# Kernel tuning notes

Hardware: AMD Instinct MI355X
Metric: run time of the kernel (lower is better)

## Reference

```python
import jax, jax.numpy as jnp
import numpy as np

EPS = 1e-12  # torch F.normalize default eps


def _l2_normalize(x):
    # normalize along last dim, matching F.normalize(dim=2)
    norm = jnp.linalg.norm(x, axis=-1, keepdims=True)
    return x / jnp.maximum(norm, EPS)


def _poly_kernel_mean(a, b):
    # mean over (B,C,C) of squared inner products along T.
    # Original does broadcast (B,1,C,T)*(B,C,1,T) then sum; einsum is the
    # efficient batched-matmul form of the same math.
    g = jnp.einsum('bct,bdt->bcd', a, b)  # (B,C,C)
    return jnp.mean(g * g)


def setup_inputs() -> dict:
    key = jax.random.key(0)
    k1, k2 = jax.random.split(key)
    B, C, T = 16, 128, 16384
    f_s = jax.random.normal(k1, (B, C, T), dtype=jnp.float32)
    f_t = jax.random.normal(k2, (B, C, T), dtype=jnp.float32)
    return {"f_s": f_s, "f_t": f_t}


def reference(f_s, f_t):
    # equal T -> no interpolation branch; view(B,C,-1) is identity for 3D
    s = _l2_normalize(f_s)
    t = _l2_normalize(f_t)
    loss = (jax.lax.stop_gradient(_poly_kernel_mean(t, t))
            + _poly_kernel_mean(s, s)
            - 2.0 * _poly_kernel_mean(s, t))
    return loss
```

## Files before the change

### kernel.cpp

```cpp
#include <hip/hip_runtime.h>
#include <hip/hip_bf16.h>

#define BATCH  16
#define CCH    128
#define TDIM   16384
#define MROWS  256
#define NCHUNK 16
#define KC     (TDIM / NCHUNK)
#define BK     32
#define NSTEP  (KC / BK)
#define PIPE   4
#define BUFFB  32768u
#define LDSBYTES (PIPE * BUFFB)
#define GRAM   (MROWS * MROWS)

typedef __attribute__((ext_vector_type(8))) short bf16x8;
typedef __attribute__((ext_vector_type(4))) float f32x4;
typedef const __attribute__((address_space(1))) unsigned int* gptr_t;
typedef __attribute__((address_space(3))) unsigned int* lptr_t;


__device__ __forceinline__ void issue_stage(
    char* smraw, const float* const (&gsrc)[4], int tid, int stage)
{
  unsigned base = (unsigned)(stage & (PIPE - 1)) * BUFFB;
  #pragma unroll
  for (int j = 0; j < 4; ++j) {
    const float* g = gsrc[j] + (size_t)stage * BK;
    char* l = smraw + base + (unsigned)(j * 512 + tid) * 16u;
    __builtin_amdgcn_global_load_lds((gptr_t)g, (lptr_t)l, 16, 0, 0);
  }
}

__device__ __forceinline__ bf16x8 frag_from_f32(const float* bp, int row, int lhi) {
  const int r7 = row & 7;
  const f32x4* pr = (const f32x4*)(bp + row * 32);
  f32x4 lo = pr[(2 * lhi)     ^ r7];
  f32x4 hi = pr[(2 * lhi + 1) ^ r7];
  union { unsigned u[4]; bf16x8 v; } o;
  asm("v_cvt_pk_bf16_f32 %0, %1, %2" : "=v"(o.u[0]) : "v"(lo.x), "v"(lo.y));
  asm("v_cvt_pk_bf16_f32 %0, %1, %2" : "=v"(o.u[1]) : "v"(lo.z), "v"(lo.w));
  asm("v_cvt_pk_bf16_f32 %0, %1, %2" : "=v"(o.u[2]) : "v"(hi.x), "v"(hi.y));
  asm("v_cvt_pk_bf16_f32 %0, %1, %2" : "=v"(o.u[3]) : "v"(hi.z), "v"(hi.w));
  return o.v;
}

__device__ __forceinline__ void compute_step(
    const float* bp, f32x4 (&acc)[4][8], int wr, int wc, int llo, int lhi)
{
  bf16x8 af[4], bfr[8];
  #pragma unroll
  for (int i = 0; i < 4; ++i)
    af[i] = frag_from_f32(bp, wr * 64 + i * 16 + llo, lhi);
  #pragma unroll
  for (int j = 0; j < 8; ++j)
    bfr[j] = frag_from_f32(bp, wc * 128 + j * 16 + llo, lhi);
  #pragma unroll
  for (int i = 0; i < 4; ++i)
    #pragma unroll
    for (int j = 0; j < 8; ++j)
      acc[i][j] = __builtin_amdgcn_mfma_f32_16x16x32_bf16(af[i], bfr[j], acc[i][j], 0, 0, 0);
}

__global__ __launch_bounds__(512, 2) void gram_kernel(
    const float* __restrict__ fs, const float* __restrict__ ft,
    float* __restrict__ outp, int atomic_mode)
{
  extern __shared__ __attribute__((aligned(16))) char smraw[];

  const int tid   = threadIdx.x;
  const int bidx  = blockIdx.x;
  const int b     = bidx / NCHUNK;
  const int chunk = bidx - b * NCHUNK;
  const int kbase = chunk * KC;

  const int lane = tid & 63;
  const int w    = tid >> 6;
  const int wr   = w & 3;
  const int wc   = w >> 2;
  const int lhi  = lane >> 4;
  const int llo  = lane & 15;

  const float* gsrc[4];
  #pragma unroll
  for (int j = 0; j < 4; ++j) {
    int idx = j * 512 + tid;
    int row = idx >> 3;
    int kq  = (idx & 7) ^ (row & 7);
    const float* base = (row < CCH)
        ? (fs + (size_t)(b * CCH + row) * TDIM)
        : (ft + (size_t)(b * CCH + (row - CCH)) * TDIM);
    gsrc[j] = base + kbase + kq * 4;
  }

  f32x4 acc[4][8];
  #pragma unroll
  for (int i = 0; i < 4; ++i)
    #pragma unroll
    for (int j = 0; j < 8; ++j)
      acc[i][j] = (f32x4){0.f, 0.f, 0.f, 0.f};

  #pragma unroll
  for (int p = 0; p < PIPE; ++p)
    issue_stage(smraw, gsrc, tid, p);

  #pragma unroll 1
  for (int s = 0; s < NSTEP; ++s) {
    if (s <= NSTEP - 4)      asm volatile("s_waitcnt vmcnt(12)" ::: "memory");
    else if (s == NSTEP - 3) asm volatile("s_waitcnt vmcnt(8)"  ::: "memory");
    else if (s == NSTEP - 2) asm volatile("s_waitcnt vmcnt(4)"  ::: "memory");
    else                     asm volatile("s_waitcnt vmcnt(0)"  ::: "memory");
    __builtin_amdgcn_s_barrier();
    asm volatile("" ::: "memory");

    const float* bp = (const float*)(smraw + (unsigned)(s & (PIPE - 1)) * BUFFB);
    compute_step(bp, acc, wr, wc, llo, lhi);

    asm volatile("s_waitcnt lgkmcnt(0)" ::: "memory");
    __builtin_amdgcn_s_barrier();
    asm volatile("" ::: "memory");

    if (s + PIPE < NSTEP)
      issue_stage(smraw, gsrc, tid, s + PIPE);
  }

  if (atomic_mode) {
    float* out = outp + (size_t)b * GRAM;
    #pragma unroll
    for (int i = 0; i < 4; ++i) {
      int row0 = wr * 64 + i * 16 + lhi * 4;
      #pragma unroll
      for (int j = 0; j < 8; ++j) {
        int col = wc * 128 + j * 16 + llo;
        #pragma unroll
        for (int r = 0; r < 4; ++r)
          atomicAdd(&out[(size_t)(row0 + r) * MROWS + col], acc[i][j][r]);
      }
    }
  } else {
    float* out = outp + (size_t)bidx * GRAM;
    #pragma unroll
    for (int i = 0; i < 4; ++i) {
      int row0 = wr * 64 + i * 16 + lhi * 4;
      #pragma unroll
      for (int j = 0; j < 8; ++j) {
        int col = wc * 128 + j * 16 + llo;
        #pragma unroll
        for (int r = 0; r < 4; ++r)
          out[(size_t)(row0 + r) * MROWS + col] = acc[i][j][r];
      }
    }
  }
}

__global__ __launch_bounds__(256) void norms_kernel(
    const float* __restrict__ gram, float* __restrict__ norms, int nchunk)
{
  int b = blockIdx.x;
  int d = threadIdx.x;
  float g = 0.f;
  int c = 0;
  for (; c + 3 < nchunk; c += 4) {
    float g0 = gram[(size_t)(b * nchunk + c + 0) * GRAM + (size_t)d * (MROWS + 1)];
    float g1 = gram[(size_t)(b * nchunk + c + 1) * GRAM + (size_t)d * (MROWS + 1)];
    float g2 = gram[(size_t)(b * nchunk + c + 2) * GRAM + (size_t)d * (MROWS + 1)];
    float g3 = gram[(size_t)(b * nchunk + c + 3) * GRAM + (size_t)d * (MROWS + 1)];
    g += (g0 + g1) + (g2 + g3);
  }
  for (; c < nchunk; ++c)
    g += gram[(size_t)(b * nchunk + c) * GRAM + (size_t)d * (MROWS + 1)];
  float n = sqrtf(fmaxf(g, 0.f));
  n = fmaxf(n, 1e-12f);
  norms[b * MROWS + d] = 1.0f / n;
}

__global__ __launch_bounds__(256) void loss_kernel(
    const float* __restrict__ gram, const float* __restrict__ norms,
    float* __restrict__ out, int nchunk)
{
  int b     = blockIdx.x >> 6;
  int strip = blockIdx.x & 63;
  int e0    = strip * 1024 + threadIdx.x * 4;
  const float* nb = norms + b * MROWS;
  const float* gp = gram + (size_t)b * nchunk * GRAM + e0;

  f32x4 g = (f32x4){0.f, 0.f, 0.f, 0.f};
  int c = 0;
  for (; c + 3 < nchunk; c += 4) {
    f32x4 v0 = *(const f32x4*)(gp + (size_t)(c + 0) * GRAM);
    f32x4 v1 = *(const f32x4*)(gp + (size_t)(c + 1) * GRAM);
    f32x4 v2 = *(const f32x4*)(gp + (size_t)(c + 2) * GRAM);
    f32x4 v3 = *(const f32x4*)(gp + (size_t)(c + 3) * GRAM);
    g += (v0 + v1) + (v2 + v3);
  }
  for (; c < nchunk; ++c)
    g += *(const f32x4*)(gp + (size_t)c * GRAM);

  int i  = e0 >> 8;
  int j0 = e0 & 255;
  float ri = nb[i];
  float accl = 0.f;
  #pragma unroll
  for (int q = 0; q < 4; ++q) {
    int j = j0 + q;
    float gh = g[q] * ri * nb[j];
    float sgn = ((i < CCH) == (j < CCH)) ? 1.f : -1.f;
    accl += sgn * gh * gh;
  }
  #pragma unroll
  for (int off = 32; off > 0; off >>= 1)
    accl += __shfl_down(accl, off, 64);
  __shared__ float red[4];
  if ((threadIdx.x & 63) == 0) red[threadIdx.x >> 6] = accl;
  __syncthreads();
  if (threadIdx.x == 0) {
    float t = red[0] + red[1] + red[2] + red[3];
    atomicAdd(out, t * (1.0f / (float)(BATCH * CCH * CCH)));
  }
}

extern "C" void kernel_launch(void* const* d_in, const int* in_sizes, int n_in,
                              void* d_out, int out_size, void* d_ws, size_t ws_size,
                              hipStream_t stream) {
  const float* fs = (const float*)d_in[0];
  const float* ft = (const float*)d_in[1];
  float* out = (float*)d_out;
  float* wsf = (float*)d_ws;

  float* norms = wsf;
  float* gram  = wsf + 4096;

  const size_t need_partials = ((size_t)4096 + (size_t)BATCH * NCHUNK * GRAM) * 4;
  const int atomic_mode = (ws_size >= need_partials) ? 0 : 1;
  const int nred = atomic_mode ? 1 : NCHUNK;

  static int lds_raised = 0;
  if (!lds_raised) {
    (void)hipFuncSetAttribute(reinterpret_cast<const void*>(gram_kernel),
                              hipFuncAttributeMaxDynamicSharedMemorySize, LDSBYTES);
    lds_raised = 1;
  }

  (void)hipMemsetAsync(d_out, 0, sizeof(float), stream);
  if (atomic_mode)
    (void)hipMemsetAsync(gram, 0, (size_t)BATCH * GRAM * sizeof(float), stream);

  gram_kernel<<<dim3(BATCH * NCHUNK), dim3(512), LDSBYTES, stream>>>(fs, ft, gram, atomic_mode);
  norms_kernel<<<dim3(BATCH), dim3(256), 0, stream>>>(gram, norms, nred);
  loss_kernel<<<dim3(BATCH * 64), dim3(256), 0, stream>>>(gram, norms, out, nred);
}
```

Measured before the change: 355.3 us.

## Stage bf16-converted tiles in LDS via register prefetch double buffering

```diff
diff --git a/kernel.cpp b/kernel.cpp
--- a/kernel.cpp
+++ b/kernel.cpp
@@ -1,5 +1,4 @@
 #include <hip/hip_runtime.h>
-#include <hip/hip_bf16.h>
 
 #define BATCH  16
 #define CCH    128
@@ -7,59 +6,58 @@
 #define MROWS  256
 #define NCHUNK 16
 #define KC     (TDIM / NCHUNK)
-#define BK     32
+#define BK     128
 #define NSTEP  (KC / BK)
-#define PIPE   4
-#define BUFFB  32768u
-#define LDSBYTES (PIPE * BUFFB)
+#define LDSH   136
+#define LDSBUF (MROWS * LDSH * 2)
+#define LDSBYTES (2 * LDSBUF)
 #define GRAM   (MROWS * MROWS)
 
 typedef __attribute__((ext_vector_type(8))) short bf16x8;
 typedef __attribute__((ext_vector_type(4))) float f32x4;
-typedef const __attribute__((address_space(1))) unsigned int* gptr_t;
-typedef __attribute__((address_space(3))) unsigned int* lptr_t;
-
-
-__device__ __forceinline__ void issue_stage(
-    char* smraw, const float* const (&gsrc)[4], int tid, int stage)
-{
-  unsigned base = (unsigned)(stage & (PIPE - 1)) * BUFFB;
-  #pragma unroll
-  for (int j = 0; j < 4; ++j) {
-    const float* g = gsrc[j] + (size_t)stage * BK;
-    char* l = smraw + base + (unsigned)(j * 512 + tid) * 16u;
-    __builtin_amdgcn_global_load_lds((gptr_t)g, (lptr_t)l, 16, 0, 0);
-  }
-}
-
-__device__ __forceinline__ bf16x8 frag_from_f32(const float* bp, int row, int lhi) {
-  const int r7 = row & 7;
-  const f32x4* pr = (const f32x4*)(bp + row * 32);
-  f32x4 lo = pr[(2 * lhi)     ^ r7];
-  f32x4 hi = pr[(2 * lhi + 1) ^ r7];
-  union { unsigned u[4]; bf16x8 v; } o;
-  asm("v_cvt_pk_bf16_f32 %0, %1, %2" : "=v"(o.u[0]) : "v"(lo.x), "v"(lo.y));
-  asm("v_cvt_pk_bf16_f32 %0, %1, %2" : "=v"(o.u[1]) : "v"(lo.z), "v"(lo.w));
-  asm("v_cvt_pk_bf16_f32 %0, %1, %2" : "=v"(o.u[2]) : "v"(hi.x), "v"(hi.y));
-  asm("v_cvt_pk_bf16_f32 %0, %1, %2" : "=v"(o.u[3]) : "v"(hi.z), "v"(hi.w));
-  return o.v;
-}
-
-__device__ __forceinline__ void compute_step(
-    const float* bp, f32x4 (&acc)[4][8], int wr, int wc, int llo, int lhi)
-{
+typedef __attribute__((ext_vector_type(4))) unsigned short u16x4;
+typedef unsigned short (*ldsrow_t)[LDSH];
+
+__device__ __forceinline__ unsigned short f2bf(float x) {
+  unsigned int u = __float_as_uint(x);
+  u += 0x7fffu + ((u >> 16) & 1u);
+  return (unsigned short)(u >> 16);
+}
+
+__device__ __forceinline__ void pipe_barrier() {
+  asm volatile("s_waitcnt lgkmcnt(0)" ::: "memory");
+  __builtin_amdgcn_s_barrier();
+  asm volatile("" ::: "memory");
+}
+
+__device__ __forceinline__ void compute_kk(
+    ldsrow_t buf, f32x4 (&acc)[4][8], int kk, int wr, int wc, int llo, int lhi)
+{
+  const int kcol = kk * 32 + lhi * 8;
   bf16x8 af[4], bfr[8];
   #pragma unroll
   for (int i = 0; i < 4; ++i)
-    af[i] = frag_from_f32(bp, wr * 64 + i * 16 + llo, lhi);
+    af[i] = *(const bf16x8*)&buf[wr * 64 + i * 16 + llo][kcol];
   #pragma unroll
   for (int j = 0; j < 8; ++j)
-    bfr[j] = frag_from_f32(bp, wc * 128 + j * 16 + llo, lhi);
+    bfr[j] = *(const bf16x8*)&buf[wc * 128 + j * 16 + llo][kcol];
   #pragma unroll
   for (int i = 0; i < 4; ++i)
     #pragma unroll
     for (int j = 0; j < 8; ++j)
       acc[i][j] = __builtin_amdgcn_mfma_f32_16x16x32_bf16(af[i], bfr[j], acc[i][j], 0, 0, 0);
+}
+
+__device__ __forceinline__ void stage_half(
+    ldsrow_t buf, const f32x4 (&v)[8], int half128, int rsub, int seg)
+{
+  #pragma unroll
+  for (int qq = 0; qq < 8; ++qq) {
+    u16x4 p;
+    p.x = f2bf(v[qq].x); p.y = f2bf(v[qq].y);
+    p.z = f2bf(v[qq].z); p.w = f2bf(v[qq].w);
+    *(u16x4*)&buf[half128 + qq * 16 + rsub][seg * 4] = p;
+  }
 }
 
 __global__ __launch_bounds__(512, 2) void gram_kernel(
@@ -67,6 +65,8 @@
     float* __restrict__ outp, int atomic_mode)
 {
   extern __shared__ __attribute__((aligned(16))) char smraw[];
+  ldsrow_t smA = (ldsrow_t)smraw;
+  ldsrow_t smB = (ldsrow_t)(smraw + LDSBUF);
 
   const int tid   = threadIdx.x;
   const int bidx  = blockIdx.x;
@@ -81,17 +81,11 @@
   const int lhi  = lane >> 4;
   const int llo  = lane & 15;
 
-  const float* gsrc[4];
-  #pragma unroll
-  for (int j = 0; j < 4; ++j) {
-    int idx = j * 512 + tid;
-    int row = idx >> 3;
-    int kq  = (idx & 7) ^ (row & 7);
-    const float* base = (row < CCH)
-        ? (fs + (size_t)(b * CCH + row) * TDIM)
-        : (ft + (size_t)(b * CCH + (row - CCH)) * TDIM);
-    gsrc[j] = base + kbase + kq * 4;
-  }
+  const int rsub = tid >> 5;
+  const int seg  = tid & 31;
+
+  const float* base_fs = fs + (size_t)(b * CCH + rsub) * TDIM + kbase + seg * 4;
+  const float* base_ft = ft + (size_t)(b * CCH + rsub) * TDIM + kbase + seg * 4;
 
   f32x4 acc[4][8];
   #pragma unroll
@@ -100,29 +94,40 @@
     for (int j = 0; j < 8; ++j)
       acc[i][j] = (f32x4){0.f, 0.f, 0.f, 0.f};
 
-  #pragma unroll
-  for (int p = 0; p < PIPE; ++p)
-    issue_stage(smraw, gsrc, tid, p);
-
+  f32x4 vA[8], vB[8];
+
+  #pragma unroll
+  for (int qq = 0; qq < 8; ++qq)
+    vA[qq] = *(const f32x4*)(base_fs + (size_t)qq * 16 * TDIM);
+  #pragma unroll
+  for (int qq = 0; qq < 8; ++qq)
+    vB[qq] = *(const f32x4*)(base_ft + (size_t)qq * 16 * TDIM);
+  stage_half(smA, vA, 0,   rsub, seg);
+  stage_half(smA, vB, 128, rsub, seg);
+  pipe_barrier();
+
+  ldsrow_t curb = smA, nxtb = smB;
   #pragma unroll 1
-  for (int s = 0; s < NSTEP; ++s) {
-    if (s <= NSTEP - 4)      asm volatile("s_waitcnt vmcnt(12)" ::: "memory");
-    else if (s == NSTEP - 3) asm volatile("s_waitcnt vmcnt(8)"  ::: "memory");
-    else if (s == NSTEP - 2) asm volatile("s_waitcnt vmcnt(4)"  ::: "memory");
-    else                     asm volatile("s_waitcnt vmcnt(0)"  ::: "memory");
-    __builtin_amdgcn_s_barrier();
-    asm volatile("" ::: "memory");
-
-    const float* bp = (const float*)(smraw + (unsigned)(s & (PIPE - 1)) * BUFFB);
-    compute_step(bp, acc, wr, wc, llo, lhi);
-
-    asm volatile("s_waitcnt lgkmcnt(0)" ::: "memory");
-    __builtin_amdgcn_s_barrier();
-    asm volatile("" ::: "memory");
-
-    if (s + PIPE < NSTEP)
-      issue_stage(smraw, gsrc, tid, s + PIPE);
-  }
+  for (int s = 0; s < NSTEP - 1; ++s) {
+    #pragma unroll
+    for (int qq = 0; qq < 8; ++qq)
+      vA[qq] = *(const f32x4*)(base_fs + (size_t)qq * 16 * TDIM + (s + 1) * BK);
+    compute_kk(curb, acc, 0, wr, wc, llo, lhi);
+    compute_kk(curb, acc, 1, wr, wc, llo, lhi);
+    #pragma unroll
+    for (int qq = 0; qq < 8; ++qq)
+      vB[qq] = *(const f32x4*)(base_ft + (size_t)qq * 16 * TDIM + (s + 1) * BK);
+    stage_half(nxtb, vA, 0, rsub, seg);
+    compute_kk(curb, acc, 2, wr, wc, llo, lhi);
+    compute_kk(curb, acc, 3, wr, wc, llo, lhi);
+    stage_half(nxtb, vB, 128, rsub, seg);
+    pipe_barrier();
+    ldsrow_t t = curb; curb = nxtb; nxtb = t;
+  }
+  compute_kk(curb, acc, 0, wr, wc, llo, lhi);
+  compute_kk(curb, acc, 1, wr, wc, llo, lhi);
+  compute_kk(curb, acc, 2, wr, wc, llo, lhi);
+  compute_kk(curb, acc, 3, wr, wc, llo, lhi);
 
   if (atomic_mode) {
     float* out = outp + (size_t)b * GRAM;
```

After: 330.7 us. 1.07x faster.
